# Kernel tuning notes

Measured on AMD Instinct MI355X. Metric: run time of the kernel, lower is better.

The kernel has to match this reference:

```python
import jax, jax.numpy as jnp
import numpy as np

N, NODES, DIN, HID, M, OUT_FE = 8192, 20000, 768, 256, 4096, 50


def setup_inputs() -> dict:
    key = jax.random.key(0)
    ks = jax.random.split(key, 12)
    s = 0.02  # small init scale to keep tanh in its linear-ish range
    return {
        "t": jax.random.normal(ks[0], (N, DIN), jnp.float32),
        "AGE_inx": jax.random.normal(ks[1], (NODES, DIN), jnp.float32),
        "Endx": jax.random.randint(ks[2], (M,), 0, NODES, jnp.int32),
        "W_age": jax.random.normal(ks[3], (DIN, DIN), jnp.float32) * s,
        "b_age": jnp.zeros((DIN,), jnp.float32),
        "W_prjT": jax.random.normal(ks[4], (HID, DIN), jnp.float32) * s,
        "b_prjT": jnp.zeros((HID,), jnp.float32),
        "W_prjL": jax.random.normal(ks[5], (HID, DIN), jnp.float32) * s,
        "b_prjL": jnp.zeros((HID,), jnp.float32),
        "outW": jax.random.normal(ks[6], (M, HID), jnp.float32) * s,
        "outb": jax.random.normal(ks[7], (M,), jnp.float32) * s,
        "W_fc3": jax.random.normal(ks[8], (OUT_FE, HID), jnp.float32) * s,
        "b_fc3": jnp.zeros((OUT_FE,), jnp.float32),
    }


def _lintrans(x, W, b):
    # AGE LinTrans: Linear -> per-row min-max scale -> L2 normalize
    z = x @ W.T + b                                   # [NODES, 768]
    zmin = jnp.min(z, axis=1, keepdims=True)
    zmax = jnp.max(z, axis=1, keepdims=True)
    z = (z - zmin) / (zmax - zmin)
    norm = jnp.sqrt(jnp.sum(z * z, axis=1, keepdims=True))
    return z / jnp.maximum(norm, 1e-12)


def reference(t, AGE_inx, Endx, W_age, b_age, W_prjT, b_prjT,
              W_prjL, b_prjL, outW, outb, W_fc3, b_fc3):
    AGE_E = _lintrans(AGE_inx, W_age, b_age)          # [NODES, 768]
    h = jnp.tanh(t @ W_prjT.T + b_prjT)               # [N, 256]
    E = jnp.tanh(AGE_E[Endx] @ W_prjL.T + b_prjL)     # [M, 256]
    # sum_d h[n,d]*E[m,d]*outW[m,d] == h @ (E*outW).T  (avoids [N,M,256] blowup)
    o_c = h @ (E * outW).T + outb                     # [N, M]
    o_f = h @ W_fc3.T + b_fc3                         # [N, OUT_FE]
    return (o_c, o_f)
```

## Files before the change

### kernel.cpp

```cpp
#include <hip/hip_runtime.h>
#include <hip/hip_bf16.h>
#include <cstdint>
#include <cstddef>

typedef __hip_bfloat16 bf16;
typedef __attribute__((ext_vector_type(4))) float f32x4;
typedef __attribute__((ext_vector_type(8))) short s16x8;

__device__ __forceinline__ void gload_lds16(const void* g, void* l) {
    __builtin_amdgcn_global_load_lds(
        (const __attribute__((address_space(1))) unsigned int*)g,
        (__attribute__((address_space(3))) unsigned int*)l,
        16, 0, 0);
}

__device__ __forceinline__ short f2bs(float x) {
    bf16 h = __float2bfloat16(x);
    return *reinterpret_cast<short*>(&h);
}

template<int TANH, int MULW, int F32OUT, int NGUARD, int ASRC, int BSRC>
__device__ __forceinline__ void gemm_body(
    short* __restrict__ sA, short* __restrict__ sB,
    int bm, int bn,
    const void* __restrict__ Aptr, const void* __restrict__ Bptr,
    const int* __restrict__ gidx,
    const float* __restrict__ bias, const float* __restrict__ Mul,
    void* __restrict__ Cout, int M, int N, int K, int ldc)
{
    const int tid  = threadIdx.x;
    const int lane = tid & 63;
    const int wave = tid >> 6;
    const int wr = wave >> 1, wc = wave & 1;
    const int l15 = lane & 15, quad = lane >> 4;

    int    slot[4];
    size_t a_off[4], b_off[4];
#pragma unroll
    for (int j = 0; j < 4; ++j) {
        int S   = (wave * 4 + j) * 64 + lane;
        int row = S >> 3;
        int cc  = (S & 7) ^ (row & 7);
        slot[j] = S * 8;
        if (ASRC == 2)
            a_off[j] = (size_t)gidx[bm * 128 + row] * K + cc * 8;
        else
            a_off[j] = (size_t)(bm * 128 + row) * K + cc * 8;
        int ng = bn * 128 + row;
        if (NGUARD) ng = (ng < N) ? ng : (N - 1);
        b_off[j] = (size_t)ng * K + cc * 8;
    }

    f32x4 acc[4][4];
#pragma unroll
    for (int i = 0; i < 4; ++i)
#pragma unroll
        for (int j = 0; j < 4; ++j)
            acc[i][j] = (f32x4){0.f, 0.f, 0.f, 0.f};

    for (int kt = 0; kt < K; kt += 64) {
#pragma unroll
        for (int j = 0; j < 4; ++j) {
            if (ASRC == 0) {
                gload_lds16((const bf16*)Aptr + a_off[j] + kt, &sA[slot[j]]);
            } else {
                const float* s = (const float*)Aptr + a_off[j] + kt;
                float4 u = *(const float4*)s;
                float4 v = *(const float4*)(s + 4);
                s16x8 p;
                p[0] = f2bs(u.x); p[1] = f2bs(u.y); p[2] = f2bs(u.z); p[3] = f2bs(u.w);
                p[4] = f2bs(v.x); p[5] = f2bs(v.y); p[6] = f2bs(v.z); p[7] = f2bs(v.w);
                *(s16x8*)&sA[slot[j]] = p;
            }
        }
#pragma unroll
        for (int j = 0; j < 4; ++j) {
            if (BSRC == 0) {
                gload_lds16((const bf16*)Bptr + b_off[j] + kt, &sB[slot[j]]);
            } else {
                const float* s = (const float*)Bptr + b_off[j] + kt;
                float4 u = *(const float4*)s;
                float4 v = *(const float4*)(s + 4);
                s16x8 p;
                p[0] = f2bs(u.x); p[1] = f2bs(u.y); p[2] = f2bs(u.z); p[3] = f2bs(u.w);
                p[4] = f2bs(v.x); p[5] = f2bs(v.y); p[6] = f2bs(v.z); p[7] = f2bs(v.w);
                *(s16x8*)&sB[slot[j]] = p;
            }
        }
        if (ASRC == 0 || BSRC == 0)
            asm volatile("s_waitcnt vmcnt(0)" ::: "memory");
        __syncthreads();

#pragma unroll
        for (int ks = 0; ks < 2; ++ks) {
            s16x8 afr[4], bfr[4];
#pragma unroll
            for (int i = 0; i < 4; ++i) {
                int r = wr * 64 + i * 16 + l15;
                int q = ks * 4 + quad;
                afr[i] = *(const s16x8*)&sA[(r * 8 + (q ^ (r & 7))) * 8];
            }
#pragma unroll
            for (int j = 0; j < 4; ++j) {
                int r = wc * 64 + j * 16 + l15;
                int q = ks * 4 + quad;
                bfr[j] = *(const s16x8*)&sB[(r * 8 + (q ^ (r & 7))) * 8];
            }
#pragma unroll
            for (int i = 0; i < 4; ++i)
#pragma unroll
                for (int j = 0; j < 4; ++j)
                    acc[i][j] = __builtin_amdgcn_mfma_f32_16x16x32_bf16(
                        afr[i], bfr[j], acc[i][j], 0, 0, 0);
        }
        __syncthreads();
    }

#pragma unroll
    for (int j = 0; j < 4; ++j) {
        int colg = bn * 128 + wc * 64 + j * 16 + l15;
        if (NGUARD && colg >= N) continue;
        float bv = bias[colg];
#pragma unroll
        for (int i = 0; i < 4; ++i) {
            int row0 = bm * 128 + wr * 64 + i * 16 + quad * 4;
#pragma unroll
            for (int r = 0; r < 4; ++r) {
                float v = acc[i][j][r] + bv;
                if (TANH) v = tanhf(v);
                if (MULW) v *= Mul[(size_t)(row0 + r) * N + colg];
                if (F32OUT)
                    ((float*)Cout)[(size_t)(row0 + r) * ldc + colg] = v;
                else
                    ((bf16*)Cout)[(size_t)(row0 + r) * ldc + colg] = __float2bfloat16(v);
            }
        }
    }
}

__global__ __launch_bounds__(256)
void mm_zh(const float* __restrict__ AGEinx, const int* __restrict__ Endx,
           const float* __restrict__ W_age, const float* __restrict__ b_age,
           float* __restrict__ z,
           const float* __restrict__ t, const float* __restrict__ W_prjT,
           const float* __restrict__ b_prjT, bf16* __restrict__ h)
{
    __shared__ short sA[128 * 64];
    __shared__ short sB[128 * 64];
    int b = blockIdx.x;
    if (b < 192) {
        gemm_body<0, 0, 1, 0, 2, 1>(sA, sB, b / 6, b % 6,
                                    AGEinx, W_age, Endx, b_age, nullptr,
                                    z, 4096, 768, 768, 768);
    } else {
        int b2 = b - 192;
        gemm_body<1, 0, 0, 0, 1, 1>(sA, sB, b2 / 2, b2 % 2,
                                    t, W_prjT, nullptr, b_prjT, nullptr,
                                    h, 8192, 256, 768, 256);
    }
}

__global__ __launch_bounds__(256)
void mm_e2(const bf16* __restrict__ AGE_E, const float* __restrict__ W_prjL,
           const float* __restrict__ b_prjL, const float* __restrict__ outW,
           bf16* __restrict__ E2)
{
    __shared__ short sA[128 * 64];
    __shared__ short sB[128 * 64];
    gemm_body<1, 1, 0, 0, 0, 1>(sA, sB, blockIdx.y, blockIdx.x,
                                AGE_E, W_prjL, nullptr, b_prjL, outW,
                                E2, 4096, 256, 768, 256);
}

__global__ __launch_bounds__(256)
void mm_out(const bf16* __restrict__ h, const bf16* __restrict__ E2,
            const float* __restrict__ outb, float* __restrict__ o_c,
            const float* __restrict__ W_fc3, const float* __restrict__ b_fc3,
            float* __restrict__ o_f)
{
    __shared__ short sA[128 * 64];
    __shared__ short sB[128 * 64];
    int b = blockIdx.x;
    if (b < 2048) {
        gemm_body<0, 0, 1, 0, 0, 0>(sA, sB, b / 32, b % 32,
                                    h, E2, nullptr, outb, nullptr,
                                    o_c, 8192, 4096, 256, 4096);
    } else {
        int b2 = b - 2048;
        gemm_body<0, 0, 1, 1, 0, 1>(sA, sB, b2, 0,
                                    h, W_fc3, nullptr, b_fc3, nullptr,
                                    o_f, 8192, 50, 256, 50);
    }
}

__global__ __launch_bounds__(256)
void lintrans_k(const float* __restrict__ z, bf16* __restrict__ out)
{
    __shared__ float rmin[4], rmax[4], rsum[4];
    const int row  = blockIdx.x;
    const int tid  = threadIdx.x;
    const int lane = tid & 63;
    const int wave = tid >> 6;
    const float* zr = z + (size_t)row * 768;

    float v0 = zr[tid], v1 = zr[tid + 256], v2 = zr[tid + 512];
    float mn = fminf(fminf(v0, v1), v2);
    float mx = fmaxf(fmaxf(v0, v1), v2);
#pragma unroll
    for (int o = 32; o > 0; o >>= 1) {
        mn = fminf(mn, __shfl_down(mn, o));
        mx = fmaxf(mx, __shfl_down(mx, o));
    }
    if (lane == 0) { rmin[wave] = mn; rmax[wave] = mx; }
    __syncthreads();
    float bmn = fminf(fminf(rmin[0], rmin[1]), fminf(rmin[2], rmin[3]));
    float bmx = fmaxf(fmaxf(rmax[0], rmax[1]), fmaxf(rmax[2], rmax[3]));
    float sc  = 1.f / (bmx - bmn);
    v0 = (v0 - bmn) * sc; v1 = (v1 - bmn) * sc; v2 = (v2 - bmn) * sc;
    float s = v0 * v0 + v1 * v1 + v2 * v2;
#pragma unroll
    for (int o = 32; o > 0; o >>= 1) s += __shfl_down(s, o);
    if (lane == 0) rsum[wave] = s;
    __syncthreads();
    float tot = rsum[0] + rsum[1] + rsum[2] + rsum[3];
    float inv = 1.f / fmaxf(sqrtf(tot), 1e-12f);
    out[(size_t)row * 768 + tid]       = __float2bfloat16(v0 * inv);
    out[(size_t)row * 768 + tid + 256] = __float2bfloat16(v1 * inv);
    out[(size_t)row * 768 + tid + 512] = __float2bfloat16(v2 * inv);
}

extern "C" void kernel_launch(void* const* d_in, const int* in_sizes, int n_in,
                              void* d_out, int out_size, void* d_ws, size_t ws_size,
                              hipStream_t stream)
{
    (void)in_sizes; (void)n_in; (void)out_size; (void)ws_size;

    const float* t_in   = (const float*)d_in[0];
    const float* AGEinx = (const float*)d_in[1];
    const int*   Endx   = (const int*)  d_in[2];
    const float* W_age  = (const float*)d_in[3];
    const float* b_age  = (const float*)d_in[4];
    const float* W_prjT = (const float*)d_in[5];
    const float* b_prjT = (const float*)d_in[6];
    const float* W_prjL = (const float*)d_in[7];
    const float* b_prjL = (const float*)d_in[8];
    const float* outW   = (const float*)d_in[9];
    const float* outb   = (const float*)d_in[10];
    const float* W_fc3  = (const float*)d_in[11];
    const float* b_fc3  = (const float*)d_in[12];

    char* ws = (char*)d_ws;
    size_t off = 0;
    float* z     = (float*)(ws + off); off += (size_t)4096 * 768 * 4;
    bf16*  h     = (bf16*) (ws + off); off += (size_t)8192 * 256 * 2;
    bf16*  AGE_E = (bf16*) (ws + off); off += (size_t)4096 * 768 * 2;
    bf16*  E2    = (bf16*) (ws + off); off += (size_t)4096 * 256 * 2;

    float* o_c = (float*)d_out;
    float* o_f = o_c + (size_t)8192 * 4096;

    mm_zh<<<320, 256, 0, stream>>>(AGEinx, Endx, W_age, b_age, z,
                                   t_in, W_prjT, b_prjT, h);
    lintrans_k<<<4096, 256, 0, stream>>>(z, AGE_E);
    mm_e2<<<dim3(2, 32), 256, 0, stream>>>(AGE_E, W_prjL, b_prjL, outW, E2);
    mm_out<<<2112, 256, 0, stream>>>(h, E2, outb, o_c, W_fc3, b_fc3, o_f);
}
```

Before: 344.5 us.

## Prefetch fp32 tiles in registers, regroup GEMM launches, swizzle output blocks

The fp32-source GEMM paths now load the next K-tile into registers while the current tile is computed, hiding global load latency. The h projection moves out of the first launch and is fused with the E2 GEMM, so the first launch only computes z and the later launch carries more blocks. The output GEMM remaps block indices so consecutive blocks share tiles for cache reuse, and h reuses z's workspace. Register pressure rises from the prefetch buffers, which could reduce occupancy.

```diff
diff --git a/kernel.cpp b/kernel.cpp
--- a/kernel.cpp
+++ b/kernel.cpp
@@ -17,6 +17,13 @@
 __device__ __forceinline__ short f2bs(float x) {
     bf16 h = __float2bfloat16(x);
     return *reinterpret_cast<short*>(&h);
+}
+
+__device__ __forceinline__ s16x8 pack8(f32x4 u, f32x4 v) {
+    s16x8 p;
+    p[0] = f2bs(u[0]); p[1] = f2bs(u[1]); p[2] = f2bs(u[2]); p[3] = f2bs(u[3]);
+    p[4] = f2bs(v[0]); p[5] = f2bs(v[1]); p[6] = f2bs(v[2]); p[7] = f2bs(v[3]);
+    return p;
 }
 
 template<int TANH, int MULW, int F32OUT, int NGUARD, int ASRC, int BSRC>
@@ -58,38 +65,61 @@
         for (int j = 0; j < 4; ++j)
             acc[i][j] = (f32x4){0.f, 0.f, 0.f, 0.f};
 
+    f32x4 pa0[4], pa1[4], pb0[4], pb1[4];
+    if (ASRC != 0) {
+#pragma unroll
+        for (int j = 0; j < 4; ++j) {
+            const float* s = (const float*)Aptr + a_off[j];
+            pa0[j] = *(const f32x4*)s;
+            pa1[j] = *(const f32x4*)(s + 4);
+        }
+    }
+    if (BSRC != 0) {
+#pragma unroll
+        for (int j = 0; j < 4; ++j) {
+            const float* s = (const float*)Bptr + b_off[j];
+            pb0[j] = *(const f32x4*)s;
+            pb1[j] = *(const f32x4*)(s + 4);
+        }
+    }
+
     for (int kt = 0; kt < K; kt += 64) {
 #pragma unroll
         for (int j = 0; j < 4; ++j) {
-            if (ASRC == 0) {
+            if (ASRC == 0)
                 gload_lds16((const bf16*)Aptr + a_off[j] + kt, &sA[slot[j]]);
-            } else {
-                const float* s = (const float*)Aptr + a_off[j] + kt;
-                float4 u = *(const float4*)s;
-                float4 v = *(const float4*)(s + 4);
-                s16x8 p;
-                p[0] = f2bs(u.x); p[1] = f2bs(u.y); p[2] = f2bs(u.z); p[3] = f2bs(u.w);
-                p[4] = f2bs(v.x); p[5] = f2bs(v.y); p[6] = f2bs(v.z); p[7] = f2bs(v.w);
-                *(s16x8*)&sA[slot[j]] = p;
-            }
-        }
-#pragma unroll
-        for (int j = 0; j < 4; ++j) {
-            if (BSRC == 0) {
+            else
+                *(s16x8*)&sA[slot[j]] = pack8(pa0[j], pa1[j]);
+        }
+#pragma unroll
+        for (int j = 0; j < 4; ++j) {
+            if (BSRC == 0)
                 gload_lds16((const bf16*)Bptr + b_off[j] + kt, &sB[slot[j]]);
-            } else {
-                const float* s = (const float*)Bptr + b_off[j] + kt;
-                float4 u = *(const float4*)s;
-                float4 v = *(const float4*)(s + 4);
-                s16x8 p;
-                p[0] = f2bs(u.x); p[1] = f2bs(u.y); p[2] = f2bs(u.z); p[3] = f2bs(u.w);
-                p[4] = f2bs(v.x); p[5] = f2bs(v.y); p[6] = f2bs(v.z); p[7] = f2bs(v.w);
-                *(s16x8*)&sB[slot[j]] = p;
-            }
+            else
+                *(s16x8*)&sB[slot[j]] = pack8(pb0[j], pb1[j]);
         }
         if (ASRC == 0 || BSRC == 0)
             asm volatile("s_waitcnt vmcnt(0)" ::: "memory");
         __syncthreads();
+
+        if (kt + 64 < K) {
+            if (ASRC != 0) {
+#pragma unroll
+                for (int j = 0; j < 4; ++j) {
+                    const float* s = (const float*)Aptr + a_off[j] + kt + 64;
+                    pa0[j] = *(const f32x4*)s;
+                    pa1[j] = *(const f32x4*)(s + 4);
+                }
+            }
+            if (BSRC != 0) {
+#pragma unroll
+                for (int j = 0; j < 4; ++j) {
+                    const float* s = (const float*)Bptr + b_off[j] + kt + 64;
+                    pb0[j] = *(const f32x4*)s;
+                    pb1[j] = *(const f32x4*)(s + 4);
+                }
+            }
+        }
 
 #pragma unroll
         for (int ks = 0; ks < 2; ++ks) {
@@ -139,37 +169,38 @@
 }
 
 __global__ __launch_bounds__(256)
-void mm_zh(const float* __restrict__ AGEinx, const int* __restrict__ Endx,
-           const float* __restrict__ W_age, const float* __restrict__ b_age,
-           float* __restrict__ z,
-           const float* __restrict__ t, const float* __restrict__ W_prjT,
-           const float* __restrict__ b_prjT, bf16* __restrict__ h)
+void mm_z(const float* __restrict__ AGEinx, const int* __restrict__ Endx,
+          const float* __restrict__ W_age, const float* __restrict__ b_age,
+          float* __restrict__ z)
 {
     __shared__ short sA[128 * 64];
     __shared__ short sB[128 * 64];
     int b = blockIdx.x;
-    if (b < 192) {
-        gemm_body<0, 0, 1, 0, 2, 1>(sA, sB, b / 6, b % 6,
-                                    AGEinx, W_age, Endx, b_age, nullptr,
-                                    z, 4096, 768, 768, 768);
-    } else {
-        int b2 = b - 192;
-        gemm_body<1, 0, 0, 0, 1, 1>(sA, sB, b2 / 2, b2 % 2,
+    gemm_body<0, 0, 1, 0, 2, 1>(sA, sB, b / 6, b % 6,
+                                AGEinx, W_age, Endx, b_age, nullptr,
+                                z, 4096, 768, 768, 768);
+}
+
+__global__ __launch_bounds__(256)
+void mm_he2(const float* __restrict__ t, const float* __restrict__ W_prjT,
+            const float* __restrict__ b_prjT, bf16* __restrict__ h,
+            const bf16* __restrict__ AGE_E, const float* __restrict__ W_prjL,
+            const float* __restrict__ b_prjL, const float* __restrict__ outW,
+            bf16* __restrict__ E2)
+{
+    __shared__ short sA[128 * 64];
+    __shared__ short sB[128 * 64];
+    int b = blockIdx.x;
+    if (b < 128) {
+        gemm_body<1, 0, 0, 0, 1, 1>(sA, sB, b / 2, b % 2,
                                     t, W_prjT, nullptr, b_prjT, nullptr,
                                     h, 8192, 256, 768, 256);
-    }
-}
-
-__global__ __launch_bounds__(256)
-void mm_e2(const bf16* __restrict__ AGE_E, const float* __restrict__ W_prjL,
-           const float* __restrict__ b_prjL, const float* __restrict__ outW,
-           bf16* __restrict__ E2)
-{
-    __shared__ short sA[128 * 64];
-    __shared__ short sB[128 * 64];
-    gemm_body<1, 1, 0, 0, 0, 1>(sA, sB, blockIdx.y, blockIdx.x,
-                                AGE_E, W_prjL, nullptr, b_prjL, outW,
-                                E2, 4096, 256, 768, 256);
+    } else {
+        int b2 = b - 128;
+        gemm_body<1, 1, 0, 0, 0, 1>(sA, sB, b2 / 2, b2 % 2,
+                                    AGE_E, W_prjL, nullptr, b_prjL, outW,
+                                    E2, 4096, 256, 768, 256);
+    }
 }
 
 __global__ __launch_bounds__(256)
@@ -182,7 +213,8 @@
     __shared__ short sB[128 * 64];
     int b = blockIdx.x;
     if (b < 2048) {
-        gemm_body<0, 0, 1, 0, 0, 0>(sA, sB, b / 32, b % 32,
+        int bs = (b & 7) * 256 + (b >> 3);
+        gemm_body<0, 0, 1, 0, 0, 0>(sA, sB, bs / 32, bs % 32,
                                     h, E2, nullptr, outb, nullptr,
                                     o_c, 8192, 4096, 256, 4096);
     } else {
@@ -251,17 +283,17 @@
 
     char* ws = (char*)d_ws;
     size_t off = 0;
-    float* z     = (float*)(ws + off); off += (size_t)4096 * 768 * 4;
-    bf16*  h     = (bf16*) (ws + off); off += (size_t)8192 * 256 * 2;
+    float* z     = (float*)(ws + off);
+    bf16*  h     = (bf16*) (ws + off); off += (size_t)4096 * 768 * 4;
     bf16*  AGE_E = (bf16*) (ws + off); off += (size_t)4096 * 768 * 2;
     bf16*  E2    = (bf16*) (ws + off); off += (size_t)4096 * 256 * 2;
 
     float* o_c = (float*)d_out;
     float* o_f = o_c + (size_t)8192 * 4096;
 
-    mm_zh<<<320, 256, 0, stream>>>(AGEinx, Endx, W_age, b_age, z,
-                                   t_in, W_prjT, b_prjT, h);
+    mm_z<<<192, 256, 0, stream>>>(AGEinx, Endx, W_age, b_age, z);
     lintrans_k<<<4096, 256, 0, stream>>>(z, AGE_E);
-    mm_e2<<<dim3(2, 32), 256, 0, stream>>>(AGE_E, W_prjL, b_prjL, outW, E2);
+    mm_he2<<<192, 256, 0, stream>>>(t_in, W_prjT, b_prjT, h,
+                                    AGE_E, W_prjL, b_prjL, outW, E2);
     mm_out<<<2112, 256, 0, stream>>>(h, E2, outb, o_c, W_fc3, b_fc3, o_f);
 }
```

Result: faster. 312.5 us (-9.3%).
